# Optimization experiments

Measured on AMD Instinct MI355X. Metric: run time of the kernel, lower is better.

## Reference

```python
import jax, jax.numpy as jnp
import numpy as np

B, C, H, W = 8, 512, 64, 64
CR = C // 16  # reduced channels = 32


def setup_inputs() -> dict:
    key = jax.random.key(0)
    ks = jax.random.split(key, 10)
    s_in = 1.0 / np.sqrt(C)
    return {
        "x": jax.random.normal(ks[0], (B, C, H, W), jnp.float32),
        "Wq": jax.random.normal(ks[1], (CR, C), jnp.float32) * s_in,
        "bq": jnp.zeros((CR,), jnp.float32),
        "Wk": jax.random.normal(ks[2], (CR, C), jnp.float32) * s_in,
        "bk": jnp.zeros((CR,), jnp.float32),
        "Wv": jax.random.normal(ks[3], (C, C), jnp.float32) * s_in,
        "bv": jnp.zeros((C,), jnp.float32),
        "Wo": jax.random.normal(ks[4], (C, C), jnp.float32) * s_in,
        "bo": jnp.zeros((C,), jnp.float32),
        "gamma": jax.random.normal(ks[5], (1,), jnp.float32) * 0.1,
    }


def reference(x, Wq, bq, Wk, bk, Wv, bv, Wo, bo, gamma):
    b, c, h, w = x.shape
    n = h * w
    xf = x.reshape(b, c, n)  # [B,C,N]; 1x1 conv == channel matmul
    q = jnp.einsum('rc,bcn->bnr', Wq, xf) + bq  # [B,N,Cr]
    k = jnp.einsum('rc,bcn->brn', Wk, xf) + bk[None, :, None]  # [B,Cr,N]
    v = jnp.einsum('oc,bcn->bon', Wv, xf) + bv[None, :, None]  # [B,C,N]
    attn = jax.nn.softmax(jnp.einsum('bnr,brm->bnm', q, k), axis=-1)  # [B,N,N]
    out = jnp.einsum('bcm,bnm->bcn', v, attn)  # value @ attn^T -> [B,C,N]
    out = jnp.einsum('oc,bcn->bon', Wo, out) + bo[None, :, None]
    out = out.reshape(b, c, h, w)
    return gamma * out + x
```

## Files before the change

### kernel.cpp

```cpp
#include <hip/hip_runtime.h>
#include <stdint.h>

typedef unsigned short u16;
typedef float f32x4 __attribute__((ext_vector_type(4)));
typedef short short8 __attribute__((ext_vector_type(8)));

__device__ __forceinline__ u16 f2bf(float f) {
  union { float f; uint32_t u; } v; v.f = f;
  return (u16)((v.u + 0x7FFFu + ((v.u >> 16) & 1u)) >> 16);
}
__device__ __forceinline__ uint32_t pack2(u16 lo, u16 hi) {
  return (uint32_t)lo | ((uint32_t)hi << 16);
}
__device__ __forceinline__ void gld_lds16(const void* gsrc, void* ldst) {
  __builtin_amdgcn_global_load_lds(
      (const __attribute__((address_space(1))) unsigned int*)gsrc,
      (__attribute__((address_space(3))) unsigned int*)ldst, 16, 0, 0);
}

#define MFMA16(a, b, c) __builtin_amdgcn_mfma_f32_16x16x32_bf16((a), (b), (c), 0, 0, 0)

__global__ void conv_w(const float* __restrict__ src, u16* __restrict__ dst, int n4) {
  int i = blockIdx.x * blockDim.x + threadIdx.x;
  if (i >= n4) return;
  float4 v = ((const float4*)src)[i];
  uint2 p;
  p.x = pack2(f2bf(v.x), f2bf(v.y));
  p.y = pack2(f2bf(v.z), f2bf(v.w));
  ((uint2*)dst)[i] = p;
}

__global__ void conv_wqk(const float* __restrict__ Wq, const float* __restrict__ Wk,
                         u16* __restrict__ dst) {
  int i = blockIdx.x * blockDim.x + threadIdx.x;
  if (i >= 8192) return;
  const float LOG2E = 1.4426950408889634f;
  bool isQ = i < 4096;
  float4 v = isQ ? ((const float4*)Wq)[i] : ((const float4*)Wk)[i - 4096];
  float s = isQ ? LOG2E : 1.0f;
  uint2 p;
  p.x = pack2(f2bf(v.x * s), f2bf(v.y * s));
  p.y = pack2(f2bf(v.z * s), f2bf(v.w * s));
  ((uint2*)dst)[i] = p;
}

__global__ __launch_bounds__(256) void qkv_proj(
    const float* __restrict__ x, const u16* __restrict__ Wvb,
    const u16* __restrict__ Wqkb, const float* __restrict__ bv,
    const float* __restrict__ bq, const float* __restrict__ bk,
    u16* __restrict__ V2, u16* __restrict__ Qb, u16* __restrict__ Kb) {
  const int b = blockIdx.y, nb = blockIdx.x * 64;
  const int oh = blockIdx.z;
  const int t = threadIdx.x, w = t >> 6, lane = t & 63, g = lane >> 4, l15 = lane & 15;
  const int wo = (w >> 1) * 32, wn = (w & 1) * 32;
  __shared__ __align__(16) u16 xT[64][64];

  f32x4 zero4 = {0.f, 0.f, 0.f, 0.f};
  f32x4 acc[4][2][2];
#pragma unroll
  for (int og = 0; og < 4; ++og)
#pragma unroll
    for (int ot = 0; ot < 2; ++ot)
#pragma unroll
      for (int nt = 0; nt < 2; ++nt) acc[og][ot][nt] = zero4;
  f32x4 accq[2][2];
  accq[0][0] = zero4; accq[0][1] = zero4; accq[1][0] = zero4; accq[1][1] = zero4;

  const int cq4 = (t >> 4) * 4, n4 = (t & 15) * 4;
  const size_t xrow = (size_t)(b * 512) * 4096 + nb + n4;

  float4 cur0 = *(const float4*)&x[xrow + (size_t)(cq4 + 0) * 4096];
  float4 cur1 = *(const float4*)&x[xrow + (size_t)(cq4 + 1) * 4096];
  float4 cur2 = *(const float4*)&x[xrow + (size_t)(cq4 + 2) * 4096];
  float4 cur3 = *(const float4*)&x[xrow + (size_t)(cq4 + 3) * 4096];

#pragma unroll
  for (int ci = 0; ci < 8; ++ci) {
    const int c0 = ci * 64;
    float4 nxt0, nxt1, nxt2, nxt3;
    if (ci < 7) {
      nxt0 = *(const float4*)&x[xrow + (size_t)(c0 + 64 + cq4 + 0) * 4096];
      nxt1 = *(const float4*)&x[xrow + (size_t)(c0 + 64 + cq4 + 1) * 4096];
      nxt2 = *(const float4*)&x[xrow + (size_t)(c0 + 64 + cq4 + 2) * 4096];
      nxt3 = *(const float4*)&x[xrow + (size_t)(c0 + 64 + cq4 + 3) * 4096];
    }
    float rr[4][4];
    rr[0][0] = cur0.x; rr[0][1] = cur0.y; rr[0][2] = cur0.z; rr[0][3] = cur0.w;
    rr[1][0] = cur1.x; rr[1][1] = cur1.y; rr[1][2] = cur1.z; rr[1][3] = cur1.w;
    rr[2][0] = cur2.x; rr[2][1] = cur2.y; rr[2][2] = cur2.z; rr[2][3] = cur2.w;
    rr[3][0] = cur3.x; rr[3][1] = cur3.y; rr[3][2] = cur3.z; rr[3][3] = cur3.w;
#pragma unroll
    for (int k = 0; k < 4; ++k) {
      int row = n4 + k;
      uint2 pk;
      pk.x = pack2(f2bf(rr[0][k]), f2bf(rr[1][k]));
      pk.y = pack2(f2bf(rr[2][k]), f2bf(rr[3][k]));
      int byte = row * 128 + ((cq4 * 2) ^ ((row & 7) << 4));
      *(uint2*)((char*)&xT[0][0] + byte) = pk;
    }
    __syncthreads();

    short8 bb[2][2];
#pragma unroll
    for (int nt = 0; nt < 2; ++nt)
#pragma unroll
      for (int ks = 0; ks < 2; ++ks) {
        int row = wn + nt * 16 + l15;
        int byte = row * 128 + (((ks * 64) + (g * 16)) ^ ((row & 7) << 4));
        bb[nt][ks] = *(const short8*)((const char*)&xT[0][0] + byte);
      }
#pragma unroll
    for (int og = 0; og < 4; ++og) {
      short8 af[2][2];
#pragma unroll
      for (int ot = 0; ot < 2; ++ot)
#pragma unroll
        for (int ks = 0; ks < 2; ++ks)
          af[ot][ks] = *(const short8*)&Wvb[(size_t)((oh * 4 + og) * 64 + wo + ot * 16 + l15) * 512 + c0 + ks * 32 + g * 8];
#pragma unroll
      for (int ks = 0; ks < 2; ++ks)
#pragma unroll
        for (int ot = 0; ot < 2; ++ot)
#pragma unroll
          for (int nt = 0; nt < 2; ++nt)
            acc[og][ot][nt] = MFMA16(af[ot][ks], bb[nt][ks], acc[og][ot][nt]);
    }
    if (oh == 0) {
      short8 aq[2][2];
#pragma unroll
      for (int ot = 0; ot < 2; ++ot)
#pragma unroll
        for (int ks = 0; ks < 2; ++ks)
          aq[ot][ks] = *(const short8*)&Wqkb[(size_t)(wo + ot * 16 + l15) * 512 + c0 + ks * 32 + g * 8];
#pragma unroll
      for (int ks = 0; ks < 2; ++ks)
#pragma unroll
        for (int ot = 0; ot < 2; ++ot)
#pragma unroll
          for (int nt = 0; nt < 2; ++nt)
            accq[ot][nt] = MFMA16(aq[ot][ks], bb[nt][ks], accq[ot][nt]);
    }
    __syncthreads();
    if (ci < 7) { cur0 = nxt0; cur1 = nxt1; cur2 = nxt2; cur3 = nxt3; }
  }

  const size_t tbase = (size_t)b * 2097152 + (size_t)(nb >> 6) * 32768;
#pragma unroll
  for (int og = 0; og < 4; ++og)
#pragma unroll
    for (int ot = 0; ot < 2; ++ot)
#pragma unroll
      for (int nt = 0; nt < 2; ++nt)
#pragma unroll
        for (int r = 0; r < 4; ++r) {
          int o = (oh * 4 + og) * 64 + wo + ot * 16 + g * 4 + r;
          int kk = wn + nt * 16 + l15;
          int swz = ((kk * 2) ^ ((o & 7) << 4)) >> 1;
          V2[tbase + o * 64 + swz] = f2bf(acc[og][ot][nt][r] + bv[o]);
        }
  if (oh == 0) {
    const float LOG2E = 1.4426950408889634f;
#pragma unroll
    for (int ot = 0; ot < 2; ++ot)
#pragma unroll
      for (int nt = 0; nt < 2; ++nt)
#pragma unroll
        for (int r = 0; r < 4; ++r) {
          int o = wo + ot * 16 + g * 4 + r;
          int n = nb + wn + nt * 16 + l15;
          if (o < 32) {
            Qb[((size_t)(b * 4096 + n)) * 32 + o] = f2bf(accq[ot][nt][r] + bq[o] * LOG2E);
          } else {
            Kb[((size_t)(b * 4096 + n)) * 32 + (o - 32)] = f2bf(accq[ot][nt][r] + bk[o - 32]);
          }
        }
  }
}

__global__ __launch_bounds__(512, 1) void attn_f(
    const u16* __restrict__ Qb, const u16* __restrict__ Kb,
    const u16* __restrict__ V2, const u16* __restrict__ Wob,
    const float* __restrict__ bo, const float* __restrict__ gamma,
    const float* __restrict__ x, float* __restrict__ out) {
  const int bid = blockIdx.x;
  const int b = bid & 7;
  const int qblk = (bid >> 3) * 128;
  const int t = threadIdx.x;
  const int w = t >> 6, lane = t & 63, g = lane >> 4, l15 = lane & 15;
  const int qg = w & 3, chh = w >> 2;
  const int qbase = qblk + qg * 32;
  const int chb = chh * 256;

  __shared__ __align__(16) u16 Vlds[2][32768];
  __shared__ __align__(16) u16 Plds[4][32][88];
  __shared__ float lsum[4][32];

  f32x4 zero4 = {0.f, 0.f, 0.f, 0.f};

  short8 qf[2];
  if (chh == 0) {
#pragma unroll
    for (int qt = 0; qt < 2; ++qt)
      qf[qt] = *(const short8*)&Qb[((size_t)(b * 4096 + qbase + qt * 16 + l15)) * 32 + g * 8];
  }

  f32x4 acc[2][16];
#pragma unroll
  for (int qt = 0; qt < 2; ++qt)
#pragma unroll
    for (int ct = 0; ct < 16; ++ct) acc[qt][ct] = zero4;
  float l_[2][4] = {{0.f, 0.f, 0.f, 0.f}, {0.f, 0.f, 0.f, 0.f}};

  const char* VBb = (const char*)(V2 + (size_t)b * 2097152);
  const size_t kb0 = (size_t)b * 4096;

  {
    const char* gsrc = VBb + w * 8192 + lane * 16;
    char* ldst = (char*)&Vlds[0][0] + w * 8192;
#pragma unroll
    for (int j = 0; j < 8; ++j) gld_lds16(gsrc + j * 1024, ldst + j * 1024);
  }
  if (chh == 0) {
    float rsv[2][4];
#pragma unroll
    for (int half = 0; half < 2; ++half) {
      short8 kfA = *(const short8*)&Kb[(kb0 + 0 + half * 32 + 0 + l15) * 32 + g * 8];
      short8 kfB = *(const short8*)&Kb[(kb0 + 0 + half * 32 + 16 + l15) * 32 + g * 8];
      f32x4 sA[2], sB[2];
      sA[0] = MFMA16(qf[0], kfA, zero4); sA[1] = MFMA16(qf[1], kfA, zero4);
      sB[0] = MFMA16(qf[0], kfB, zero4); sB[1] = MFMA16(qf[1], kfB, zero4);
#pragma unroll
      for (int qt = 0; qt < 2; ++qt)
#pragma unroll
        for (int r = 0; r < 4; ++r) {
          float pA = exp2f(sA[qt][r]), pB = exp2f(sB[qt][r]);
          Plds[qg][qt * 16 + g * 4 + r][(half * 2 + 0) * 16 + l15] = f2bf(pA);
          Plds[qg][qt * 16 + g * 4 + r][(half * 2 + 1) * 16 + l15] = f2bf(pB);
          float v = pA + pB;
          rsv[qt][r] = half ? (rsv[qt][r] + v) : v;
        }
    }
#pragma unroll
    for (int qt = 0; qt < 2; ++qt)
#pragma unroll
      for (int r = 0; r < 4; ++r) {
        float rs = rsv[qt][r];
        rs += __shfl_xor(rs, 1);
        rs += __shfl_xor(rs, 2);
        rs += __shfl_xor(rs, 4);
        rs += __shfl_xor(rs, 8);
        l_[qt][r] += rs;
      }
  }
  asm volatile("s_waitcnt vmcnt(0) lgkmcnt(0)" ::: "memory");
  __builtin_amdgcn_s_barrier();
  __builtin_amdgcn_sched_barrier(0);

  for (int kv = 0; kv < 4096; kv += 64) {
    const int buf = (kv >> 6) & 1;
    const bool more = (kv + 64) < 4096;

    if (more) {
      const char* gsrc = VBb + (size_t)((kv >> 6) + 1) * 65536 + w * 8192 + lane * 16;
      char* ldst = (char*)&Vlds[buf ^ 1][0] + w * 8192;
#pragma unroll
      for (int j = 0; j < 8; ++j) gld_lds16(gsrc + j * 1024, ldst + j * 1024);
    }

    short8 pf[2][2];
#pragma unroll
    for (int qt = 0; qt < 2; ++qt)
#pragma unroll
      for (int k2 = 0; k2 < 2; ++k2)
        pf[qt][k2] = *(const short8*)&Plds[qg][qt * 16 + l15][k2 * 32 + g * 8];

    asm volatile("s_waitcnt lgkmcnt(0)" ::: "memory");
    __builtin_amdgcn_s_barrier();
    __builtin_amdgcn_sched_barrier(0);

    if (chh == 0 && more) {
      float rsv[2][4];
#pragma unroll
      for (int half = 0; half < 2; ++half) {
        short8 kfA = *(const short8*)&Kb[(kb0 + kv + 64 + half * 32 + 0 + l15) * 32 + g * 8];
        short8 kfB = *(const short8*)&Kb[(kb0 + kv + 64 + half * 32 + 16 + l15) * 32 + g * 8];
        f32x4 sA[2], sB[2];
        sA[0] = MFMA16(qf[0], kfA, zero4); sA[1] = MFMA16(qf[1], kfA, zero4);
        sB[0] = MFMA16(qf[0], kfB, zero4); sB[1] = MFMA16(qf[1], kfB, zero4);
#pragma unroll
        for (int qt = 0; qt < 2; ++qt)
#pragma unroll
          for (int r = 0; r < 4; ++r) {
            float pA = exp2f(sA[qt][r]), pB = exp2f(sB[qt][r]);
            Plds[qg][qt * 16 + g * 4 + r][(half * 2 + 0) * 16 + l15] = f2bf(pA);
            Plds[qg][qt * 16 + g * 4 + r][(half * 2 + 1) * 16 + l15] = f2bf(pB);
            float v = pA + pB;
            rsv[qt][r] = half ? (rsv[qt][r] + v) : v;
          }
      }
#pragma unroll
      for (int qt = 0; qt < 2; ++qt)
#pragma unroll
        for (int r = 0; r < 4; ++r) {
          float rs = rsv[qt][r];
          rs += __shfl_xor(rs, 1);
          rs += __shfl_xor(rs, 2);
          rs += __shfl_xor(rs, 4);
          rs += __shfl_xor(rs, 8);
          l_[qt][r] += rs;
        }
    }

#pragma unroll
    for (int ct = 0; ct < 16; ++ct) {
      int c = chb + ct * 16 + l15;
      int sw = (c & 7) << 4;
      const char* vrow = (const char*)&Vlds[buf][0] + c * 128;
      short8 vf0 = *(const short8*)(vrow + ((g * 16) ^ sw));
      short8 vf1 = *(const short8*)(vrow + ((64 + g * 16) ^ sw));
      acc[0][ct] = MFMA16(pf[0][0], vf0, acc[0][ct]);
      acc[0][ct] = MFMA16(pf[0][1], vf1, acc[0][ct]);
      acc[1][ct] = MFMA16(pf[1][0], vf0, acc[1][ct]);
      acc[1][ct] = MFMA16(pf[1][1], vf1, acc[1][ct]);
    }

    asm volatile("s_waitcnt vmcnt(0) lgkmcnt(0)" ::: "memory");
    __builtin_amdgcn_s_barrier();
    __builtin_amdgcn_sched_barrier(0);
  }

  if (chh == 0 && l15 == 0) {
#pragma unroll
    for (int qt = 0; qt < 2; ++qt)
#pragma unroll
      for (int r = 0; r < 4; ++r)
        lsum[qg][qt * 16 + g * 4 + r] = l_[qt][r];
  }
  __syncthreads();

  u16* AO = (u16*)&Vlds[0][0];
#pragma unroll
  for (int qt = 0; qt < 2; ++qt) {
    float inv[4];
#pragma unroll
    for (int r = 0; r < 4; ++r) inv[r] = 1.0f / lsum[qg][qt * 16 + g * 4 + r];
#pragma unroll
    for (int ct = 0; ct < 16; ++ct)
#pragma unroll
      for (int r = 0; r < 4; ++r) {
        int nrow = qg * 32 + qt * 16 + g * 4 + r;
        int c = chb + ct * 16 + l15;
        AO[nrow * 512 + (c ^ ((nrow & 7) << 3))] = f2bf(acc[qt][ct][r] * inv[r]);
      }
  }
  __syncthreads();

  f32x4 oacc[4][8];
#pragma unroll
  for (int ot = 0; ot < 4; ++ot)
#pragma unroll
    for (int nt = 0; nt < 8; ++nt) oacc[ot][nt] = zero4;

  for (int c0 = 0; c0 < 512; c0 += 64) {
#pragma unroll
    for (int nth = 0; nth < 2; ++nth) {
      short8 bb[4][2];
#pragma unroll
      for (int n2 = 0; n2 < 4; ++n2)
#pragma unroll
        for (int ks = 0; ks < 2; ++ks) {
          int row = (nth * 4 + n2) * 16 + l15;
          int coff = (c0 + ks * 32 + g * 8) ^ ((row & 7) << 3);
          bb[n2][ks] = *(const short8*)&AO[row * 512 + coff];
        }
#pragma unroll
      for (int ot = 0; ot < 4; ++ot) {
        short8 af[2];
#pragma unroll
        for (int ks = 0; ks < 2; ++ks)
          af[ks] = *(const short8*)&Wob[(size_t)(w * 64 + ot * 16 + l15) * 512 + c0 + ks * 32 + g * 8];
#pragma unroll
        for (int ks = 0; ks < 2; ++ks)
#pragma unroll
          for (int n2 = 0; n2 < 4; ++n2)
            oacc[ot][nth * 4 + n2] = MFMA16(af[ks], bb[n2][ks], oacc[ot][nth * 4 + n2]);
      }
    }
  }

  float gm = gamma[0];
#pragma unroll
  for (int ot = 0; ot < 4; ++ot)
#pragma unroll
    for (int nt = 0; nt < 8; ++nt)
#pragma unroll
      for (int r = 0; r < 4; ++r) {
        int o = w * 64 + ot * 16 + g * 4 + r;
        int n = qblk + nt * 16 + l15;
        size_t idx = ((size_t)(b * 512 + o)) * 4096 + n;
        out[idx] = gm * (oacc[ot][nt][r] + bo[o]) + x[idx];
      }
}

extern "C" void kernel_launch(void* const* d_in, const int* in_sizes, int n_in,
                              void* d_out, int out_size, void* d_ws, size_t ws_size,
                              hipStream_t stream) {
  (void)in_sizes; (void)n_in; (void)out_size; (void)ws_size;
  const float* x     = (const float*)d_in[0];
  const float* Wq    = (const float*)d_in[1];
  const float* bq    = (const float*)d_in[2];
  const float* Wk    = (const float*)d_in[3];
  const float* bk    = (const float*)d_in[4];
  const float* Wv    = (const float*)d_in[5];
  const float* bv    = (const float*)d_in[6];
  const float* Wo    = (const float*)d_in[7];
  const float* bo    = (const float*)d_in[8];
  const float* gamma = (const float*)d_in[9];

  char* wsb = (char*)d_ws;
  u16* V2   = (u16*)(wsb + 0);
  u16* Qb   = (u16*)(wsb + (size_t)33554432);
  u16* Kb   = (u16*)(wsb + (size_t)35651584);
  u16* Wvb  = (u16*)(wsb + (size_t)37748736);
  u16* Wob  = (u16*)(wsb + (size_t)38273024);
  u16* Wqkb = (u16*)(wsb + (size_t)38797312);

  conv_w<<<256, 256, 0, stream>>>(Wv, Wvb, 65536);
  conv_w<<<256, 256, 0, stream>>>(Wo, Wob, 65536);
  conv_wqk<<<32, 256, 0, stream>>>(Wq, Wk, Wqkb);
  qkv_proj<<<dim3(64, 8, 2), 256, 0, stream>>>(x, Wvb, Wqkb, bv, bq, bk, V2, Qb, Kb);
  attn_f<<<256, 512, 0, stream>>>(Qb, Kb, V2, Wob, bo, gamma, x, (float*)d_out);
}
```

Measured before the change: 329.5 us.

## Double-buffer softmax P tile to drop mid-loop barrier; merge weight conversion kernels

The P (probability) tile in LDS is now double-buffered and XOR-swizzled, so the next block's QK^T/exp results go into the other buffer. This removes the mid-iteration barrier that separated reading P from writing the next P. K fragments are prefetched before the P reads, and the two halves of score computation are merged into one batch of eight MFMAs. The three weight-conversion kernels are fused into one launch. The cost is more LDS for the second P buffer, with lsum now aliased into it, and more registers live at once.

```diff
diff --git a/kernel.cpp b/kernel.cpp
--- a/kernel.cpp
+++ b/kernel.cpp
@@ -20,28 +20,32 @@
 
 #define MFMA16(a, b, c) __builtin_amdgcn_mfma_f32_16x16x32_bf16((a), (b), (c), 0, 0, 0)
 
-__global__ void conv_w(const float* __restrict__ src, u16* __restrict__ dst, int n4) {
+__global__ void conv_all(const float* __restrict__ Wv, const float* __restrict__ Wo,
+                         const float* __restrict__ Wq, const float* __restrict__ Wk,
+                         u16* __restrict__ Wvb, u16* __restrict__ Wob,
+                         u16* __restrict__ Wqkb) {
   int i = blockIdx.x * blockDim.x + threadIdx.x;
-  if (i >= n4) return;
-  float4 v = ((const float4*)src)[i];
-  uint2 p;
-  p.x = pack2(f2bf(v.x), f2bf(v.y));
-  p.y = pack2(f2bf(v.z), f2bf(v.w));
-  ((uint2*)dst)[i] = p;
-}
-
-__global__ void conv_wqk(const float* __restrict__ Wq, const float* __restrict__ Wk,
-                         u16* __restrict__ dst) {
-  int i = blockIdx.x * blockDim.x + threadIdx.x;
-  if (i >= 8192) return;
+  if (i >= 139264) return;
   const float LOG2E = 1.4426950408889634f;
-  bool isQ = i < 4096;
-  float4 v = isQ ? ((const float4*)Wq)[i] : ((const float4*)Wk)[i - 4096];
-  float s = isQ ? LOG2E : 1.0f;
+  float4 v;
+  u16* dst;
+  int di;
+  float s = 1.0f;
+  if (i < 65536) {
+    v = ((const float4*)Wv)[i]; dst = Wvb; di = i;
+  } else if (i < 131072) {
+    v = ((const float4*)Wo)[i - 65536]; dst = Wob; di = i - 65536;
+  } else {
+    int j = i - 131072;
+    bool isQ = j < 4096;
+    v = isQ ? ((const float4*)Wq)[j] : ((const float4*)Wk)[j - 4096];
+    s = isQ ? LOG2E : 1.0f;
+    dst = Wqkb; di = j;
+  }
   uint2 p;
   p.x = pack2(f2bf(v.x * s), f2bf(v.y * s));
   p.y = pack2(f2bf(v.z * s), f2bf(v.w * s));
-  ((uint2*)dst)[i] = p;
+  ((uint2*)dst)[di] = p;
 }
 
 __global__ __launch_bounds__(256) void qkv_proj(
@@ -192,8 +196,7 @@
   const int chb = chh * 256;
 
   __shared__ __align__(16) u16 Vlds[2][32768];
-  __shared__ __align__(16) u16 Plds[4][32][88];
-  __shared__ float lsum[4][32];
+  __shared__ __align__(16) u16 P2[2][4][32][64];
 
   f32x4 zero4 = {0.f, 0.f, 0.f, 0.f};
 
@@ -234,8 +237,10 @@
 #pragma unroll
         for (int r = 0; r < 4; ++r) {
           float pA = exp2f(sA[qt][r]), pB = exp2f(sB[qt][r]);
-          Plds[qg][qt * 16 + g * 4 + r][(half * 2 + 0) * 16 + l15] = f2bf(pA);
-          Plds[qg][qt * 16 + g * 4 + r][(half * 2 + 1) * 16 + l15] = f2bf(pB);
+          int row = qt * 16 + g * 4 + r;
+          int x8 = (row & 7) << 3;
+          P2[0][qg][row][((half * 2 + 0) * 16 + l15) ^ x8] = f2bf(pA);
+          P2[0][qg][row][((half * 2 + 1) * 16 + l15) ^ x8] = f2bf(pB);
           float v = pA + pB;
           rsv[qt][r] = half ? (rsv[qt][r] + v) : v;
         }
@@ -267,42 +272,43 @@
       for (int j = 0; j < 8; ++j) gld_lds16(gsrc + j * 1024, ldst + j * 1024);
     }
 
+    short8 kfA, kfB, kfC, kfD;
+    if (chh == 0 && more) {
+      kfA = *(const short8*)&Kb[(kb0 + kv + 64 + 0 + l15) * 32 + g * 8];
+      kfB = *(const short8*)&Kb[(kb0 + kv + 64 + 16 + l15) * 32 + g * 8];
+      kfC = *(const short8*)&Kb[(kb0 + kv + 64 + 32 + l15) * 32 + g * 8];
+      kfD = *(const short8*)&Kb[(kb0 + kv + 64 + 48 + l15) * 32 + g * 8];
+    }
+
     short8 pf[2][2];
 #pragma unroll
-    for (int qt = 0; qt < 2; ++qt)
+    for (int qt = 0; qt < 2; ++qt) {
+      int row = qt * 16 + l15;
+      int x8 = (l15 & 7) << 3;
 #pragma unroll
       for (int k2 = 0; k2 < 2; ++k2)
-        pf[qt][k2] = *(const short8*)&Plds[qg][qt * 16 + l15][k2 * 32 + g * 8];
-
-    asm volatile("s_waitcnt lgkmcnt(0)" ::: "memory");
-    __builtin_amdgcn_s_barrier();
-    __builtin_amdgcn_sched_barrier(0);
+        pf[qt][k2] = *(const short8*)&P2[buf][qg][row][(k2 * 32 + g * 8) ^ x8];
+    }
 
     if (chh == 0 && more) {
-      float rsv[2][4];
-#pragma unroll
-      for (int half = 0; half < 2; ++half) {
-        short8 kfA = *(const short8*)&Kb[(kb0 + kv + 64 + half * 32 + 0 + l15) * 32 + g * 8];
-        short8 kfB = *(const short8*)&Kb[(kb0 + kv + 64 + half * 32 + 16 + l15) * 32 + g * 8];
-        f32x4 sA[2], sB[2];
-        sA[0] = MFMA16(qf[0], kfA, zero4); sA[1] = MFMA16(qf[1], kfA, zero4);
-        sB[0] = MFMA16(qf[0], kfB, zero4); sB[1] = MFMA16(qf[1], kfB, zero4);
-#pragma unroll
-        for (int qt = 0; qt < 2; ++qt)
-#pragma unroll
-          for (int r = 0; r < 4; ++r) {
-            float pA = exp2f(sA[qt][r]), pB = exp2f(sB[qt][r]);
-            Plds[qg][qt * 16 + g * 4 + r][(half * 2 + 0) * 16 + l15] = f2bf(pA);
-            Plds[qg][qt * 16 + g * 4 + r][(half * 2 + 1) * 16 + l15] = f2bf(pB);
-            float v = pA + pB;
-            rsv[qt][r] = half ? (rsv[qt][r] + v) : v;
-          }
-      }
+      f32x4 sA[2], sB[2], sC[2], sD[2];
+      sA[0] = MFMA16(qf[0], kfA, zero4); sA[1] = MFMA16(qf[1], kfA, zero4);
+      sB[0] = MFMA16(qf[0], kfB, zero4); sB[1] = MFMA16(qf[1], kfB, zero4);
+      sC[0] = MFMA16(qf[0], kfC, zero4); sC[1] = MFMA16(qf[1], kfC, zero4);
+      sD[0] = MFMA16(qf[0], kfD, zero4); sD[1] = MFMA16(qf[1], kfD, zero4);
 #pragma unroll
       for (int qt = 0; qt < 2; ++qt)
 #pragma unroll
         for (int r = 0; r < 4; ++r) {
-          float rs = rsv[qt][r];
+          float pA = exp2f(sA[qt][r]), pB = exp2f(sB[qt][r]);
+          float pC = exp2f(sC[qt][r]), pD = exp2f(sD[qt][r]);
+          int row = qt * 16 + g * 4 + r;
+          int x8 = (row & 7) << 3;
+          P2[buf ^ 1][qg][row][(0 * 16 + l15) ^ x8] = f2bf(pA);
+          P2[buf ^ 1][qg][row][(1 * 16 + l15) ^ x8] = f2bf(pB);
+          P2[buf ^ 1][qg][row][(2 * 16 + l15) ^ x8] = f2bf(pC);
+          P2[buf ^ 1][qg][row][(3 * 16 + l15) ^ x8] = f2bf(pD);
+          float rs = (pA + pB) + (pC + pD);
           rs += __shfl_xor(rs, 1);
           rs += __shfl_xor(rs, 2);
           rs += __shfl_xor(rs, 4);
@@ -329,12 +335,13 @@
     __builtin_amdgcn_sched_barrier(0);
   }
 
+  float* lsum = (float*)&P2[0][0][0][0];
   if (chh == 0 && l15 == 0) {
 #pragma unroll
     for (int qt = 0; qt < 2; ++qt)
 #pragma unroll
       for (int r = 0; r < 4; ++r)
-        lsum[qg][qt * 16 + g * 4 + r] = l_[qt][r];
+        lsum[qg * 32 + qt * 16 + g * 4 + r] = l_[qt][r];
   }
   __syncthreads();
 
@@ -343,7 +350,7 @@
   for (int qt = 0; qt < 2; ++qt) {
     float inv[4];
 #pragma unroll
-    for (int r = 0; r < 4; ++r) inv[r] = 1.0f / lsum[qg][qt * 16 + g * 4 + r];
+    for (int r = 0; r < 4; ++r) inv[r] = 1.0f / lsum[qg * 32 + qt * 16 + g * 4 + r];
 #pragma unroll
     for (int ct = 0; ct < 16; ++ct)
 #pragma unroll
@@ -425,9 +432,7 @@
   u16* Wob  = (u16*)(wsb + (size_t)38273024);
   u16* Wqkb = (u16*)(wsb + (size_t)38797312);
 
-  conv_w<<<256, 256, 0, stream>>>(Wv, Wvb, 65536);
-  conv_w<<<256, 256, 0, stream>>>(Wo, Wob, 65536);
-  conv_wqk<<<32, 256, 0, stream>>>(Wq, Wk, Wqkb);
+  conv_all<<<544, 256, 0, stream>>>(Wv, Wo, Wq, Wk, Wvb, Wob, Wqkb);
   qkv_proj<<<dim3(64, 8, 2), 256, 0, stream>>>(x, Wvb, Wqkb, bv, bq, bk, V2, Qb, Kb);
   attn_f<<<256, 512, 0, stream>>>(Qb, Kb, V2, Wob, bo, gamma, x, (float*)d_out);
 }
```

Measured after the change: 347.4 us. 5.4% more time.
